# Kernel optimization log

Measured on AMD Instinct MI355X. Metric: run time of the kernel, lower is better.

## Reference

```python
import jax, jax.numpy as jnp
import numpy as np

EPS = 1e-5
QMAX = 127.0


def fake_quant_int8(x):
    """Per-tensor symmetric int8 fake-quant (quantize+dequantize), dynamic scale.
    Mirrors brevitas Int8ActPerTensorFloat / Int8WeightPerTensorFloat math."""
    scale = jnp.maximum(jnp.max(jnp.abs(x)) / QMAX, 1e-8)
    q = jnp.clip(jnp.round(x / scale), -128.0, 127.0) * scale
    # straight-through estimator (identity grad through quant)
    return x + jax.lax.stop_gradient(q - x)


def layer_norm(x, g, b):
    mu = jnp.mean(x, axis=-1, keepdims=True)
    var = jnp.mean(jnp.square(x - mu), axis=-1, keepdims=True)
    return (x - mu) * jax.lax.rsqrt(var + EPS) * g + b


def setup_inputs() -> dict:
    key = jax.random.key(0)
    B, S, D, H = 64, 196, 768, 12
    M = 4 * D
    ks = jax.random.split(key, 8)
    s = lambda d: 1.0 / np.sqrt(d)
    return {
        "x": jax.random.normal(ks[0], (B, S, D), jnp.float32),
        "ln1_g": jnp.ones((D,), jnp.float32),
        "ln1_b": jnp.zeros((D,), jnp.float32),
        "ln2_g": jnp.ones((D,), jnp.float32),
        "ln2_b": jnp.zeros((D,), jnp.float32),
        "w_qkv": jax.random.normal(ks[1], (D, 3 * D), jnp.float32) * s(D),
        "b_qkv": jnp.zeros((3 * D,), jnp.float32),
        "w_o": jax.random.normal(ks[2], (D, D), jnp.float32) * s(D),
        "b_o": jnp.zeros((D,), jnp.float32),
        "w1": jax.random.normal(ks[3], (D, M), jnp.float32) * s(D),
        "b1": jnp.zeros((M,), jnp.float32),
        "w2": jax.random.normal(ks[4], (M, D), jnp.float32) * s(M),
        "b2": jnp.zeros((D,), jnp.float32),
    }


def _block(x, ln1_g, ln1_b, ln2_g, ln2_b, w_qkv, b_qkv, w_o, b_o, w1, b1, w2, b2):
    B, S, D = x.shape
    H = 12
    hd = D // H

    # --- LN -> quant -> MHSA -> add ---
    r1 = x
    h = fake_quant_int8(layer_norm(x, ln1_g, ln1_b))
    qkv = jnp.einsum("bsd,de->bse", h, fake_quant_int8(w_qkv)) + b_qkv
    q, k, v = jnp.split(qkv, 3, axis=-1)
    q = q.reshape(B, S, H, hd)
    k = k.reshape(B, S, H, hd)
    v = v.reshape(B, S, H, hd)
    logits = jnp.einsum("bqhd,bkhd->bhqk", q, k) / jnp.sqrt(jnp.float32(hd))
    attn = jax.nn.softmax(logits, axis=-1)
    ctx = jnp.einsum("bhqk,bkhd->bqhd", attn, v).reshape(B, S, D)
    ctx = fake_quant_int8(ctx)
    mhsa = jnp.einsum("bsd,de->bse", ctx, fake_quant_int8(w_o)) + b_o
    x = mhsa + r1

    # --- LN -> quant -> MLP (fc1 -> GELU -> quant -> fc2) -> add ---
    r2 = x
    h = fake_quant_int8(layer_norm(x, ln2_g, ln2_b))
    h = jnp.einsum("bsd,dm->bsm", h, fake_quant_int8(w1)) + b1
    h = jax.nn.gelu(h, approximate=False)  # torch nn.GELU default = exact erf
    h = fake_quant_int8(h)
    h = jnp.einsum("bsm,md->bsd", h, fake_quant_int8(w2)) + b2
    return h + r2


def reference(x, ln1_g, ln1_b, ln2_g, ln2_b, w_qkv, b_qkv, w_o, b_o, w1, b1, w2, b2):
    return _block(x, ln1_g, ln1_b, ln2_g, ln2_b, w_qkv, b_qkv, w_o, b_o, w1, b1, w2, b2)
```

## Files before the change

### kernel.cpp

```cpp
#include <hip/hip_runtime.h>
#include <cstdint>
#include <cstddef>

#define DEVFN __device__ __forceinline__

typedef short bf16x8 __attribute__((ext_vector_type(8)));
typedef float f32x4  __attribute__((ext_vector_type(4)));
typedef int   i32x4  __attribute__((ext_vector_type(4)));

static constexpr int NTOK  = 64 * 196;
static constexpr int DMODEL= 768;
static constexpr int NHEAD = 12;
static constexpr int NQKV  = 2304;
static constexpr int MMLP  = 3072;
static constexpr int SEQ   = 196;
static constexpr int NBATCH= 64;

enum { SL_LN1=0, SL_WQKV=1, SL_CTX=2, SL_WO=3, SL_LN2=4, SL_W1=5, SL_GELU=6, SL_W2=7 };

static constexpr int NSH       = 64;
static constexpr int SH_STRIDE = 64;
static constexpr int SLOTS_U32 = NSH * SH_STRIDE;

DEVFN float bf2f(unsigned short u){ return __uint_as_float(((unsigned)u) << 16); }
DEVFN unsigned cvt_pk_bf16(float a, float b){
  unsigned r;
  asm("v_cvt_pk_bf16_f32 %0, %1, %2" : "=v"(r) : "v"(a), "v"(b));
  return r;
}
DEVFN void split_pk(float a, float b, unsigned& hp, unsigned& lp){
  hp = cvt_pk_bf16(a, b);
  float ra = a - __uint_as_float(hp << 16);
  float rb = b - __uint_as_float(hp & 0xffff0000u);
  lp = cvt_pk_bf16(ra, rb);
}
DEVFN float slot_absmax(const unsigned* __restrict__ slots, int slot){
  unsigned m = 0u;
#pragma unroll
  for (int j = 0; j < NSH; j++){
    unsigned u = slots[j * SH_STRIDE + slot];
    m = (u > m) ? u : m;
  }
  return __uint_as_float(m);
}
DEVFN float slot_scale(const unsigned* __restrict__ slots, int slot){
  return fmaxf(slot_absmax(slots, slot) / 127.0f, 1e-8f);
}
DEVFN void scatter_amax(unsigned* slots, int slot, unsigned bucket, float v){
  atomicMax(slots + (bucket & (NSH - 1)) * SH_STRIDE + slot, __float_as_uint(v));
}
DEVFN float quantval(float x, float s){
  float q = rintf(x / s);
  return fminf(fmaxf(q, -128.0f), 127.0f);
}
DEVFN unsigned pack4(float a, float b, float c, float d){
  return  ((unsigned)(unsigned char)(char)(int)a)
        | ((unsigned)(unsigned char)(char)(int)b << 8)
        | ((unsigned)(unsigned char)(char)(int)c << 16)
        | ((unsigned)(unsigned char)(char)(int)d << 24);
}
DEVFN float gelu_fast(float v){
  float s  = v * 0.70710678118654752f;
  float ax = fabsf(s);
  float t  = __builtin_amdgcn_rcpf(fmaf(0.3275911f, ax, 1.0f));
  float p  = t * fmaf(t, fmaf(t, fmaf(t, fmaf(t, 1.061405429f, -1.453152027f),
                                      1.421413741f), -0.284496736f), 0.254829592f);
  float er = fmaf(-p, __expf(-ax * ax), 1.0f);
  unsigned sgn = __float_as_uint(s) & 0x80000000u;
  er = __uint_as_float(__float_as_uint(er) | sgn);
  return 0.5f * v * (1.0f + er);
}
DEVFN f32x4 mfma16(bf16x8 a, bf16x8 b, f32x4 c){
  return __builtin_amdgcn_mfma_f32_16x16x32_bf16(a, b, c, 0, 0, 0);
}
DEVFN i32x4 mfma16i8(i32x4 a, i32x4 b, i32x4 c){
  return __builtin_amdgcn_mfma_i32_16x16x64_i8(a, b, c, 0, 0, 0);
}
DEVFN void async_ld16(const void* g, void* lds){
  __builtin_amdgcn_global_load_lds((const __attribute__((address_space(1))) void*)g,
                                   (__attribute__((address_space(3))) void*)lds, 16, 0, 0);
}
DEVFN int vidx(int d, int s){
  return d * 256 + (s ^ (((d ^ (d >> 2)) & 7) << 3));
}
DEVFN void xcd_swizzle(int gx, int gy, int& bx, int& by){
  int nwg = gx * gy;
  int bid = blockIdx.y * gx + blockIdx.x;
  int q = nwg >> 3, r = nwg & 7;
  int xcd = bid & 7, loc = bid >> 3;
  int sw = (xcd < r) ? (xcd * (q + 1) + loc) : (r * (q + 1) + (xcd - r) * q + loc);
  bx = sw % gx; by = sw / gx;
}

DEVFN float ln_stats_wave(const float* __restrict__ x, const float* __restrict__ g,
                          const float* __restrict__ b, float2* __restrict__ stats,
                          int row, int lane){
  const float4* xr = (const float4*)(x + (size_t)row * DMODEL);
  float4 v[3];
  float sum = 0.f;
#pragma unroll
  for (int i = 0; i < 3; i++){ v[i] = xr[i * 64 + lane]; sum += v[i].x + v[i].y + v[i].z + v[i].w; }
  for (int off = 32; off; off >>= 1) sum += __shfl_xor(sum, off);
  float mu = sum * (1.0f / 768.0f);
  float vs = 0.f;
#pragma unroll
  for (int i = 0; i < 3; i++){
    float dx = v[i].x - mu, dy = v[i].y - mu, dz = v[i].z - mu, dw = v[i].w - mu;
    vs += dx * dx + dy * dy + dz * dz + dw * dw;
  }
  for (int off = 32; off; off >>= 1) vs += __shfl_xor(vs, off);
  float inv = 1.0f / sqrtf(vs * (1.0f / 768.0f) + 1e-5f);
  const float4* g4 = (const float4*)g; const float4* b4 = (const float4*)b;
  float am = 0.f;
#pragma unroll
  for (int i = 0; i < 3; i++){
    float4 gg = g4[i * 64 + lane], bb = b4[i * 64 + lane];
    float ox = (v[i].x - mu) * inv * gg.x + bb.x;
    float oy = (v[i].y - mu) * inv * gg.y + bb.y;
    float oz = (v[i].z - mu) * inv * gg.z + bb.z;
    float ow = (v[i].w - mu) * inv * gg.w + bb.w;
    am = fmaxf(am, fmaxf(fmaxf(fabsf(ox), fabsf(oy)), fmaxf(fabsf(oz), fabsf(ow))));
  }
  if (lane == 0) stats[row] = float2{mu, inv};
  return am;
}
DEVFN void ln_quant_wave(const float* __restrict__ x, const float* __restrict__ g,
                         const float* __restrict__ b, const float2* __restrict__ stats,
                         char* __restrict__ outq, float s, int row, int lane){
  float2 st = stats[row];
  float mu = st.x, inv = st.y;
  const float4* xr = (const float4*)(x + (size_t)row * DMODEL);
  const float4* g4 = (const float4*)g; const float4* b4 = (const float4*)b;
  unsigned* oq = (unsigned*)(outq + (size_t)row * DMODEL);
#pragma unroll
  for (int i = 0; i < 3; i++){
    float4 v = xr[i * 64 + lane];
    float4 gg = g4[i * 64 + lane], bb = b4[i * 64 + lane];
    float ox = (v.x - mu) * inv * gg.x + bb.x;
    float oy = (v.y - mu) * inv * gg.y + bb.y;
    float oz = (v.z - mu) * inv * gg.z + bb.z;
    float ow = (v.w - mu) * inv * gg.w + bb.w;
    oq[i * 64 + lane] = pack4(quantval(ox, s), quantval(oy, s),
                              quantval(oz, s), quantval(ow, s));
  }
}

__global__ void k_ln_stats(const float* __restrict__ x, const float* __restrict__ g,
                           const float* __restrict__ b, float2* __restrict__ stats,
                           unsigned* slots, int slot){
  int w = threadIdx.x >> 6, lane = threadIdx.x & 63;
  int row = blockIdx.x * 4 + w;
  float am = ln_stats_wave(x, g, b, stats, row, lane);
  for (int off = 32; off; off >>= 1) am = fmaxf(am, __shfl_xor(am, off));
  __shared__ float am4[4];
  if (lane == 0) am4[w] = am;
  __syncthreads();
  if (threadIdx.x == 0){
    float bm = fmaxf(fmaxf(am4[0], am4[1]), fmaxf(am4[2], am4[3]));
    scatter_amax(slots, slot, blockIdx.x, bm);
  }
}
__global__ void k_ln_quant(const float* __restrict__ x, const float* __restrict__ g,
                           const float* __restrict__ b, const float2* __restrict__ stats,
                           char* __restrict__ outq, const unsigned* __restrict__ slots, int slot){
  int w = threadIdx.x >> 6, lane = threadIdx.x & 63;
  int row = blockIdx.x * 4 + w;
  float s = slot_scale(slots, slot);
  ln_quant_wave(x, g, b, stats, outq, s, row, lane);
}

__global__ void k_prep1(const float* __restrict__ w_qkv, const float* __restrict__ w_o,
                        const float* __restrict__ w1, const float* __restrict__ w2,
                        const float* __restrict__ x, const float* __restrict__ g,
                        const float* __restrict__ b, float2* __restrict__ stats,
                        unsigned* slots){
  __shared__ float red[4];
  int bid = blockIdx.x;
  int lane = threadIdx.x & 63, w = threadIdx.x >> 6;
  if (bid < 896){
    const float* xx; int n4, slot, b0, nb;
    if (bid < 256)      { xx = w_qkv; n4 = DMODEL * NQKV  / 4; slot = SL_WQKV; b0 = 0;   nb = 256; }
    else if (bid < 384) { xx = w_o;   n4 = DMODEL * DMODEL/ 4; slot = SL_WO;   b0 = 256; nb = 128; }
    else if (bid < 640) { xx = w1;    n4 = DMODEL * MMLP  / 4; slot = SL_W1;   b0 = 384; nb = 256; }
    else                { xx = w2;    n4 = MMLP   * DMODEL/ 4; slot = SL_W2;   b0 = 640; nb = 256; }
    int lb = bid - b0;
    float m = 0.f;
    const float4* x4 = (const float4*)xx;
    int stride = nb * blockDim.x;
    for (int j = lb * blockDim.x + threadIdx.x; j < n4; j += stride){
      float4 v = x4[j];
      m = fmaxf(m, fmaxf(fmaxf(fabsf(v.x), fabsf(v.y)), fmaxf(fabsf(v.z), fabsf(v.w))));
    }
    for (int off = 32; off; off >>= 1) m = fmaxf(m, __shfl_xor(m, off));
    if (lane == 0) red[w] = m;
    __syncthreads();
    if (threadIdx.x == 0){
      float bm = fmaxf(fmaxf(red[0], red[1]), fmaxf(red[2], red[3]));
      scatter_amax(slots, slot, bid, bm);
    }
  } else {
    int row = (bid - 896) * 4 + w;
    float am = ln_stats_wave(x, g, b, stats, row, lane);
    for (int off = 32; off; off >>= 1) am = fmaxf(am, __shfl_xor(am, off));
    if (lane == 0) red[w] = am;
    __syncthreads();
    if (threadIdx.x == 0){
      float bm = fmaxf(fmaxf(red[0], red[1]), fmaxf(red[2], red[3]));
      scatter_amax(slots, SL_LN1, bid, bm);
    }
  }
}

__global__ void k_prep2(const float* __restrict__ w0, const float* __restrict__ w1,
                        const float* __restrict__ w2, const float* __restrict__ w3,
                        char* __restrict__ t0, char* __restrict__ t1,
                        char* __restrict__ t2, char* __restrict__ t3,
                        const float* __restrict__ x, const float* __restrict__ g,
                        const float* __restrict__ b, const float2* __restrict__ stats,
                        char* __restrict__ outq, const unsigned* __restrict__ slots){
  __shared__ float tile[32][33];
  int bid = blockIdx.x;
  if (bid < 6912){
    const float* w; char* wt; int K, N, slot, lb;
    if (bid < 1728)      { w = w0; wt = t0; K = DMODEL; N = NQKV;   slot = SL_WQKV; lb = bid; }
    else if (bid < 2304) { w = w1; wt = t1; K = DMODEL; N = DMODEL; slot = SL_WO;   lb = bid - 1728; }
    else if (bid < 4608) { w = w2; wt = t2; K = DMODEL; N = MMLP;   slot = SL_W1;   lb = bid - 2304; }
    else                 { w = w3; wt = t3; K = MMLP;   N = DMODEL; slot = SL_W2;   lb = bid - 4608; }
    int nx = N / 32;
    int bx = lb % nx, by = lb / nx;
    float s = slot_scale(slots, slot);
    int n0 = bx * 32, k0 = by * 32;
    int tx = threadIdx.x & 31, ty = threadIdx.x >> 5;
#pragma unroll
    for (int i = 0; i < 4; i++){
      int k = k0 + ty + i * 8;
      float v = w[(size_t)k * N + n0 + tx];
      tile[ty + i * 8][tx] = quantval(v, s);
    }
    __syncthreads();
    int n = threadIdx.x >> 3, kg = threadIdx.x & 7;
    unsigned o = pack4(tile[kg * 4 + 0][n], tile[kg * 4 + 1][n],
                       tile[kg * 4 + 2][n], tile[kg * 4 + 3][n]);
    *(unsigned*)(wt + (size_t)(n0 + n) * K + k0 + kg * 4) = o;
  } else {
    int w = threadIdx.x >> 6, lane = threadIdx.x & 63;
    int row = (bid - 6912) * 4 + w;
    float s = slot_scale(slots, SL_LN1);
    ln_quant_wave(x, g, b, stats, outq, s, row, lane);
  }
}

__global__ void k_quant_act(const float* __restrict__ x, unsigned* __restrict__ out,
                            int n4, const unsigned* __restrict__ slots, int slot){
  float s = slot_scale(slots, slot);
  const float4* x4 = (const float4*)x;
  int stride = gridDim.x * blockDim.x;
  for (int j = blockIdx.x * blockDim.x + threadIdx.x; j < n4; j += stride){
    float4 v = x4[j];
    out[j] = pack4(quantval(v.x, s), quantval(v.y, s), quantval(v.z, s), quantval(v.w, s));
  }
}

__global__ void k_quant_bf16_i8(const unsigned short* __restrict__ x, unsigned* __restrict__ out,
                                int n4, const unsigned* __restrict__ slots, int slot){
  float s = slot_scale(slots, slot);
  const ushort4* x4 = (const ushort4*)x;
  int stride = gridDim.x * blockDim.x;
  for (int j = blockIdx.x * blockDim.x + threadIdx.x; j < n4; j += stride){
    ushort4 v = x4[j];
    out[j] = pack4(quantval(bf2f(v.x), s), quantval(bf2f(v.y), s),
                   quantval(bf2f(v.z), s), quantval(bf2f(v.w), s));
  }
}

template<int EPI>
__launch_bounds__(256, 4)
__global__ void k_gemm(const char* __restrict__ A,
                       const char* __restrict__ Bt,
                       const float* __restrict__ bias,
                       const float* __restrict__ res,
                       float* __restrict__ Cf,
                       unsigned short* __restrict__ Cb,
                       const unsigned* __restrict__ slots, int sa_slot, int sb_slot,
                       unsigned* gmax_slots, int gmax_slot,
                       int M, int N, int K)
{
  __shared__ __align__(16) char smem[32768];
  __shared__ float gm4[4];
  const int tid  = threadIdx.x;
  const int lane = tid & 63;
  const int wv   = tid >> 6;
  const int wx   = wv & 1, wy = wv >> 1;
  const int quad = lane >> 4;
  const int l16  = lane & 15;
  int bx, by;
  xcd_swizzle(gridDim.x, gridDim.y, bx, by);
  const int m0 = by * 128, n0 = bx * 128;

  auto issue = [&](int k0, int buf){
#pragma unroll
    for (int i = 0; i < 2; i++){
      int c = tid + i * 256;
      int row = c >> 2, q = c & 3;
      int qs = (q - ((row + (row >> 2)) & 3)) & 3;
      async_ld16(A + (size_t)(m0 + row) * K + k0 + qs * 16,
                 smem + buf * 8192 + (i * 256 + wv * 64) * 16);
    }
#pragma unroll
    for (int i = 0; i < 2; i++){
      int c = tid + i * 256;
      int row = c >> 2, q = c & 3;
      int qs = (q - ((row + (row >> 2)) & 3)) & 3;
      async_ld16(Bt + (size_t)(n0 + row) * K + k0 + qs * 16,
                 smem + 16384 + buf * 8192 + (i * 256 + wv * 64) * 16);
    }
  };

  i32x4 acc[4][4] = {};
  const int nk = K >> 6;
  issue(0, 0);

  const int ch = (((quad + (l16 & 3) + (l16 >> 2)) & 3)) * 16;

  for (int k = 0; k < nk; k++){
    const int cur = k & 1;
    if (k + 1 < nk){
      issue((k + 1) << 6, cur ^ 1);
      asm volatile("s_waitcnt vmcnt(4)" ::: "memory");
    } else {
      asm volatile("s_waitcnt vmcnt(0)" ::: "memory");
    }
    asm volatile("s_barrier" ::: "memory");

    const char* Ab = smem + cur * 8192;
    const char* Bb = smem + 16384 + cur * 8192;
    i32x4 af[4], bfr[4];
#pragma unroll
    for (int i = 0; i < 4; i++)
      af[i] = *(const i32x4*)(Ab + (wy * 64 + i * 16 + l16) * 64 + ch);
#pragma unroll
    for (int j = 0; j < 4; j++)
      bfr[j] = *(const i32x4*)(Bb + (wx * 64 + j * 16 + l16) * 64 + ch);
    asm volatile("s_waitcnt lgkmcnt(0)" ::: "memory");
    asm volatile("s_barrier" ::: "memory");

#pragma unroll
    for (int i = 0; i < 4; i++)
#pragma unroll
      for (int j = 0; j < 4; j++)
        acc[i][j] = mfma16i8(af[i], bfr[j], acc[i][j]);
  }
  __syncthreads();

  float (*stage)[132] = (float (*)[132])smem;
  const float sc = slot_scale(slots, sa_slot) * slot_scale(slots, sb_slot);
  const int col4 = (tid & 31) * 4;
  const int gc   = n0 + col4;
  const float4 bb = *(const float4*)&bias[gc];
  float gmax = 0.f;
#pragma unroll
  for (int i = 0; i < 4; i++){
#pragma unroll
    for (int j = 0; j < 4; j++)
#pragma unroll
      for (int r = 0; r < 4; r++)
        stage[wy * 16 + quad * 4 + r][wx * 64 + j * 16 + l16] = (float)acc[i][j][r];
    __syncthreads();
#pragma unroll
    for (int rr = 0; rr < 4; rr++){
      const int rl = rr * 8 + (tid >> 5);
      const int gm = m0 + ((rl >> 4) * 64) + i * 16 + (rl & 15);
      float4 v = *(const float4*)&stage[rl][col4];
      v.x = v.x * sc + bb.x; v.y = v.y * sc + bb.y;
      v.z = v.z * sc + bb.z; v.w = v.w * sc + bb.w;
      if constexpr (EPI == 1){
        float4 rv = *(const float4*)&res[(size_t)gm * N + gc];
        v.x += rv.x; v.y += rv.y; v.z += rv.z; v.w += rv.w;
        *(float4*)&Cf[(size_t)gm * N + gc] = v;
      } else if constexpr (EPI == 2){
        float g0 = gelu_fast(v.x);
        float g1 = gelu_fast(v.y);
        float g2 = gelu_fast(v.z);
        float g3 = gelu_fast(v.w);
        gmax = fmaxf(gmax, fmaxf(fmaxf(fabsf(g0), fabsf(g1)), fmaxf(fabsf(g2), fabsf(g3))));
        uint2 o = {cvt_pk_bf16(g0, g1), cvt_pk_bf16(g2, g3)};
        *(uint2*)&Cb[(size_t)gm * N + gc] = o;
      } else {
        *(float4*)&Cf[(size_t)gm * N + gc] = v;
      }
    }
    __syncthreads();
  }
  if constexpr (EPI == 2){
    for (int off = 32; off; off >>= 1) gmax = fmaxf(gmax, __shfl_xor(gmax, off));
    if (lane == 0) gm4[wv] = gmax;
    __syncthreads();
    if (tid == 0){
      float bm = fmaxf(fmaxf(gm4[0], gm4[1]), fmaxf(gm4[2], gm4[3]));
      scatter_amax(gmax_slots, gmax_slot, blockIdx.x + blockIdx.y * gridDim.x, bm);
    }
  }
}

__launch_bounds__(832, 4)
__global__ void k_attention(const float* __restrict__ qkv, float* __restrict__ ctx,
                            unsigned* slots){
  __shared__ __align__(16) unsigned short Khi[208 * 72], Klo[208 * 72];
  __shared__ __align__(16) unsigned short Vhi[64 * 256], Vlo[64 * 256];
  __shared__ __align__(16) unsigned short Ps[13][2][16 * 40];
  __shared__ float gm[13];

  const int bh = ((blockIdx.x & 7) * 96) + (blockIdx.x >> 3);
  const int b = bh / NHEAD, h = bh % NHEAD;
  const float* base = qkv + (size_t)b * SEQ * NQKV;
  const int tid = threadIdx.x, lane = tid & 63, wv = tid >> 6;
  const int quad = lane >> 4, l16 = lane & 15;

  float4 kreg[4], vreg[5];
#pragma unroll
  for (int i = 0; i < 4; i++){
    int idx = tid + i * 832;
    int r = idx >> 4, c4 = (idx & 15) * 4;
    float4 v = {0.f, 0.f, 0.f, 0.f};
    if (r < SEQ) v = *(const float4*)(base + (size_t)r * NQKV + DMODEL + h * 64 + c4);
    kreg[i] = v;
  }
#pragma unroll
  for (int i = 0; i < 5; i++){
    int idx = tid + i * 832;
    int s = idx >> 4, dg = (idx & 15) * 4;
    float4 v = {0.f, 0.f, 0.f, 0.f};
    if (idx < 232 * 16 && s < SEQ)
      v = *(const float4*)(base + (size_t)s * NQKV + 2 * DMODEL + h * 64 + dg);
    vreg[i] = v;
  }
#pragma unroll
  for (int i = 0; i < 4; i++){
    int idx = tid + i * 832;
    int r = idx >> 4, c4 = (idx & 15) * 4;
    float4 v = kreg[i];
    unsigned h01, l01, h23, l23;
    split_pk(v.x, v.y, h01, l01);
    split_pk(v.z, v.w, h23, l23);
    *(uint2*)(Khi + r * 72 + c4) = uint2{h01, h23};
    *(uint2*)(Klo + r * 72 + c4) = uint2{l01, l23};
  }
#pragma unroll
  for (int i = 0; i < 5; i++){
    int idx = tid + i * 832;
    if (idx < 232 * 16){
      int s = idx >> 4, dg = (idx & 15) * 4;
      float4 v = vreg[i];
      unsigned h01, l01, h23, l23;
      split_pk(v.x, v.y, h01, l01);
      split_pk(v.z, v.w, h23, l23);
      Vhi[vidx(dg + 0, s)] = (unsigned short)h01; Vhi[vidx(dg + 1, s)] = (unsigned short)(h01 >> 16);
      Vhi[vidx(dg + 2, s)] = (unsigned short)h23; Vhi[vidx(dg + 3, s)] = (unsigned short)(h23 >> 16);
      Vlo[vidx(dg + 0, s)] = (unsigned short)l01; Vlo[vidx(dg + 1, s)] = (unsigned short)(l01 >> 16);
      Vlo[vidx(dg + 2, s)] = (unsigned short)l23; Vlo[vidx(dg + 3, s)] = (unsigned short)(l23 >> 16);
    }
  }
  __syncthreads();

  unsigned short* PsH = &Ps[wv][0][0];
  unsigned short* PsL = &Ps[wv][1][0];

  float gmax = 0.f;
  const int qt = wv;
  {
    const int q0 = qt * 16;
    const int sq = q0 + l16;
    const bool valid = sq < SEQ;

    bf16x8 aqh[2], aql[2];
    const float* qrow = base + (size_t)(valid ? sq : 0) * NQKV + h * 64;
#pragma unroll
    for (int ks = 0; ks < 2; ks++){
      float4 v0 = {0,0,0,0}, v1 = {0,0,0,0};
      if (valid){
        v0 = *(const float4*)(qrow + ks * 32 + quad * 8);
        v1 = *(const float4*)(qrow + ks * 32 + quad * 8 + 4);
      }
      unsigned* ah = (unsigned*)&aqh[ks];
      unsigned* al = (unsigned*)&aql[ks];
      split_pk(v0.x, v0.y, ah[0], al[0]);
      split_pk(v0.z, v0.w, ah[1], al[1]);
      split_pk(v1.x, v1.y, ah[2], al[2]);
      split_pk(v1.z, v1.w, ah[3], al[3]);
    }

    f32x4 sacc[13];
    __builtin_amdgcn_s_setprio(1);
#pragma unroll
    for (int t = 0; t < 13; t++){
      f32x4 a = {0.f, 0.f, 0.f, 0.f};
#pragma unroll
      for (int ks = 0; ks < 2; ks++){
        bf16x8 bkh = *(const bf16x8*)(Khi + (t * 16 + l16) * 72 + ks * 32 + quad * 8);
        bf16x8 bkl = *(const bf16x8*)(Klo + (t * 16 + l16) * 72 + ks * 32 + quad * 8);
        a = mfma16(aqh[ks], bkh, a);
        a = mfma16(aqh[ks], bkl, a);
        a = mfma16(aql[ks], bkh, a);
      }
      sacc[t] = a;
    }
    __builtin_amdgcn_s_setprio(0);

    float mx[4] = {-1e30f, -1e30f, -1e30f, -1e30f};
#pragma unroll
    for (int t = 0; t < 13; t++){
      bool dead = (t == 12) && (l16 >= 4);
#pragma unroll
      for (int r = 0; r < 4; r++){
        float v = dead ? -1e30f : sacc[t][r] * 0.125f;
        sacc[t][r] = v;
        mx[r] = fmaxf(mx[r], v);
      }
    }
#pragma unroll
    for (int off = 1; off < 16; off <<= 1)
#pragma unroll
      for (int r = 0; r < 4; r++) mx[r] = fmaxf(mx[r], __shfl_xor(mx[r], off));
    float sum[4] = {0.f, 0.f, 0.f, 0.f};
#pragma unroll
    for (int t = 0; t < 13; t++)
#pragma unroll
      for (int r = 0; r < 4; r++){
        float e = __expf(sacc[t][r] - mx[r]);
        sacc[t][r] = e; sum[r] += e;
      }
#pragma unroll
    for (int off = 1; off < 16; off <<= 1)
#pragma unroll
      for (int r = 0; r < 4; r++) sum[r] += __shfl_xor(sum[r], off);
    float inv[4];
#pragma unroll
    for (int r = 0; r < 4; r++) inv[r] = 1.0f / sum[r];

    f32x4 oacc[4] = {};
#pragma unroll
    for (int ks = 0; ks < 7; ks++){
      const int t0 = 2 * ks, t1 = 2 * ks + 1;
#pragma unroll
      for (int r = 0; r < 4; r++){
        int row = quad * 4 + r;
        float a = sacc[t0][r] * inv[r];
        float c = (t1 < 13) ? sacc[t1][r] * inv[r] : 0.f;
        unsigned hp, lp;
        split_pk(a, c, hp, lp);
        PsH[row * 40 + l16]      = (unsigned short)hp;
        PsH[row * 40 + 16 + l16] = (unsigned short)(hp >> 16);
        PsL[row * 40 + l16]      = (unsigned short)lp;
        PsL[row * 40 + 16 + l16] = (unsigned short)(lp >> 16);
      }
      __builtin_amdgcn_wave_barrier();
      bf16x8 aph = *(const bf16x8*)(PsH + l16 * 40 + quad * 8);
      bf16x8 apl = *(const bf16x8*)(PsL + l16 * 40 + quad * 8);
      __builtin_amdgcn_s_setprio(1);
#pragma unroll
      for (int n = 0; n < 4; n++){
        bf16x8 bvh = *(const bf16x8*)(Vhi + vidx(n * 16 + l16, ks * 32 + quad * 8));
        bf16x8 bvl = *(const bf16x8*)(Vlo + vidx(n * 16 + l16, ks * 32 + quad * 8));
        oacc[n] = mfma16(aph, bvh, oacc[n]);
        oacc[n] = mfma16(aph, bvl, oacc[n]);
        oacc[n] = mfma16(apl, bvh, oacc[n]);
      }
      __builtin_amdgcn_s_setprio(0);
      __builtin_amdgcn_wave_barrier();
    }

#pragma unroll
    for (int r = 0; r < 4; r++){
      int srow = q0 + quad * 4 + r;
      if (srow < SEQ){
#pragma unroll
        for (int n = 0; n < 4; n++){
          float v = oacc[n][r];
          ctx[((size_t)(b * SEQ + srow)) * DMODEL + h * 64 + n * 16 + l16] = v;
          gmax = fmaxf(gmax, fabsf(v));
        }
      }
    }
  }
  for (int off = 32; off; off >>= 1) gmax = fmaxf(gmax, __shfl_xor(gmax, off));
  if (lane == 0) gm[wv] = gmax;
  __syncthreads();
  if (tid == 0){
    float bm = 0.f;
#pragma unroll
    for (int i = 0; i < 13; i++) bm = fmaxf(bm, gm[i]);
    scatter_amax(slots, SL_CTX, blockIdx.x, bm);
  }
}

extern "C" void kernel_launch(void* const* d_in, const int* in_sizes, int n_in,
                              void* d_out, int out_size, void* d_ws, size_t ws_size,
                              hipStream_t stream)
{
  const float* x     = (const float*)d_in[0];
  const float* ln1_g = (const float*)d_in[1];
  const float* ln1_b = (const float*)d_in[2];
  const float* ln2_g = (const float*)d_in[3];
  const float* ln2_b = (const float*)d_in[4];
  const float* w_qkv = (const float*)d_in[5];
  const float* b_qkv = (const float*)d_in[6];
  const float* w_o   = (const float*)d_in[7];
  const float* b_o   = (const float*)d_in[8];
  const float* w1    = (const float*)d_in[9];
  const float* b1    = (const float*)d_in[10];
  const float* w2    = (const float*)d_in[11];
  const float* b2    = (const float*)d_in[12];

  char* ws = (char*)d_ws;
  size_t off = 0;
  unsigned* slots = (unsigned*)ws;                 off += SLOTS_U32 * 4;
  float2* stats = (float2*)(ws + off);             off += (size_t)NTOK * 8;
  char* wqkvT = (char*)(ws + off); off += (size_t)NQKV  * DMODEL;
  char* woT   = (char*)(ws + off); off += (size_t)DMODEL* DMODEL;
  char* w1T   = (char*)(ws + off); off += (size_t)MMLP  * DMODEL;
  char* w2T   = (char*)(ws + off); off += (size_t)DMODEL* MMLP;
  off = (off + 255) & ~(size_t)255;
  float* t1    = (float*)(ws + off);               off += (size_t)NTOK * DMODEL * 4;
  char*  t1q   = (char*)(ws + off);                off += (size_t)NTOK * DMODEL;
  off = (off + 255) & ~(size_t)255;
  float* qkv   = (float*)(ws + off);               off += (size_t)NTOK * NQKV * 4;
  float* xmid  = (float*)(ws + off);               off += (size_t)NTOK * DMODEL * 4;
  unsigned short* h1 = (unsigned short*)qkv;
  char* h1q = (char*)qkv + (size_t)NTOK * MMLP * 2;
  float* outp = (float*)d_out;

  hipMemsetAsync(slots, 0, SLOTS_U32 * 4, stream);

  k_prep1<<<4032, 256, 0, stream>>>(w_qkv, w_o, w1, w2, x, ln1_g, ln1_b, stats, slots);
  k_prep2<<<10048, 256, 0, stream>>>(w_qkv, w_o, w1, w2, wqkvT, woT, w1T, w2T,
                                     x, ln1_g, ln1_b, stats, t1q, slots);

  k_gemm<0><<<dim3(NQKV / 128, NTOK / 128), 256, 0, stream>>>(
      t1q, wqkvT, b_qkv, nullptr, qkv, nullptr, slots, SL_LN1, SL_WQKV, nullptr, 0,
      NTOK, NQKV, DMODEL);

  k_attention<<<NBATCH * NHEAD, 832, 0, stream>>>(qkv, t1, slots);
  {
    int n4 = NTOK * DMODEL / 4;
    k_quant_act<<<2048, 256, 0, stream>>>(t1, (unsigned*)t1q, n4, slots, SL_CTX);
  }
  k_gemm<1><<<dim3(DMODEL / 128, NTOK / 128), 256, 0, stream>>>(
      t1q, woT, b_o, x, xmid, nullptr, slots, SL_CTX, SL_WO, nullptr, 0,
      NTOK, DMODEL, DMODEL);

  k_ln_stats<<<NTOK / 4, 256, 0, stream>>>(xmid, ln2_g, ln2_b, stats, slots, SL_LN2);
  k_ln_quant<<<NTOK / 4, 256, 0, stream>>>(xmid, ln2_g, ln2_b, stats, t1q, slots, SL_LN2);

  k_gemm<2><<<dim3(MMLP / 128, NTOK / 128), 256, 0, stream>>>(
      t1q, w1T, b1, nullptr, nullptr, h1, slots, SL_LN2, SL_W1, slots, SL_GELU,
      NTOK, MMLP, DMODEL);
  {
    int n4 = NTOK * MMLP / 4;
    k_quant_bf16_i8<<<2048, 256, 0, stream>>>(h1, (unsigned*)h1q, n4, slots, SL_GELU);
  }
  k_gemm<1><<<dim3(DMODEL / 128, NTOK / 128), 256, 0, stream>>>(
      h1q, w2T, b2, xmid, outp, nullptr, slots, SL_GELU, SL_W2, nullptr, 0,
      NTOK, DMODEL, MMLP);
}
```

Baseline: 432.8 us.

## Fuse activation int8 quantization into GEMM A-operand load path

Removes the two standalone quantization kernels (fp32 ctx -> int8 and bf16 GELU output -> int8). The out-projection and fc2 GEMMs now load the raw fp32 or bf16 activations into registers, quantize and pack them to int8, and store them into the swizzled shared-memory A tile, while B is still loaded asynchronously. This saves a full write and re-read of the int8 intermediates and two kernel launches. In exchange the A global reads grow (4x for fp32, 2x for bf16, re-read once per N-tile column), the A path goes through registers instead of async loads, and register pressure rises.

```diff
diff --git a/kernel.cpp b/kernel.cpp
--- a/kernel.cpp
+++ b/kernel.cpp
@@ -250,30 +250,7 @@
   }
 }
 
-__global__ void k_quant_act(const float* __restrict__ x, unsigned* __restrict__ out,
-                            int n4, const unsigned* __restrict__ slots, int slot){
-  float s = slot_scale(slots, slot);
-  const float4* x4 = (const float4*)x;
-  int stride = gridDim.x * blockDim.x;
-  for (int j = blockIdx.x * blockDim.x + threadIdx.x; j < n4; j += stride){
-    float4 v = x4[j];
-    out[j] = pack4(quantval(v.x, s), quantval(v.y, s), quantval(v.z, s), quantval(v.w, s));
-  }
-}
-
-__global__ void k_quant_bf16_i8(const unsigned short* __restrict__ x, unsigned* __restrict__ out,
-                                int n4, const unsigned* __restrict__ slots, int slot){
-  float s = slot_scale(slots, slot);
-  const ushort4* x4 = (const ushort4*)x;
-  int stride = gridDim.x * blockDim.x;
-  for (int j = blockIdx.x * blockDim.x + threadIdx.x; j < n4; j += stride){
-    ushort4 v = x4[j];
-    out[j] = pack4(quantval(bf2f(v.x), s), quantval(bf2f(v.y), s),
-                   quantval(bf2f(v.z), s), quantval(bf2f(v.w), s));
-  }
-}
-
-template<int EPI>
+template<int EPI, int ASRC>
 __launch_bounds__(256, 4)
 __global__ void k_gemm(const char* __restrict__ A,
                        const char* __restrict__ Bt,
@@ -297,7 +274,17 @@
   xcd_swizzle(gridDim.x, gridDim.y, bx, by);
   const int m0 = by * 128, n0 = bx * 128;
 
-  auto issue = [&](int k0, int buf){
+  auto issueB = [&](int k0, int buf){
+#pragma unroll
+    for (int i = 0; i < 2; i++){
+      int c = tid + i * 256;
+      int row = c >> 2, q = c & 3;
+      int qs = (q - ((row + (row >> 2)) & 3)) & 3;
+      async_ld16(Bt + (size_t)(n0 + row) * K + k0 + qs * 16,
+                 smem + 16384 + buf * 8192 + (i * 256 + wv * 64) * 16);
+    }
+  };
+  auto issueA_async = [&](int k0, int buf){
 #pragma unroll
     for (int i = 0; i < 2; i++){
       int c = tid + i * 256;
@@ -306,49 +293,125 @@
       async_ld16(A + (size_t)(m0 + row) * K + k0 + qs * 16,
                  smem + buf * 8192 + (i * 256 + wv * 64) * 16);
     }
-#pragma unroll
-    for (int i = 0; i < 2; i++){
-      int c = tid + i * 256;
-      int row = c >> 2, q = c & 3;
-      int qs = (q - ((row + (row >> 2)) & 3)) & 3;
-      async_ld16(Bt + (size_t)(n0 + row) * K + k0 + qs * 16,
-                 smem + 16384 + buf * 8192 + (i * 256 + wv * 64) * 16);
-    }
   };
 
   i32x4 acc[4][4] = {};
   const int nk = K >> 6;
-  issue(0, 0);
-
   const int ch = (((quad + (l16 & 3) + (l16 >> 2)) & 3)) * 16;
 
-  for (int k = 0; k < nk; k++){
-    const int cur = k & 1;
-    if (k + 1 < nk){
-      issue((k + 1) << 6, cur ^ 1);
-      asm volatile("s_waitcnt vmcnt(4)" ::: "memory");
-    } else {
-      asm volatile("s_waitcnt vmcnt(0)" ::: "memory");
-    }
-    asm volatile("s_barrier" ::: "memory");
-
-    const char* Ab = smem + cur * 8192;
-    const char* Bb = smem + 16384 + cur * 8192;
-    i32x4 af[4], bfr[4];
-#pragma unroll
-    for (int i = 0; i < 4; i++)
-      af[i] = *(const i32x4*)(Ab + (wy * 64 + i * 16 + l16) * 64 + ch);
-#pragma unroll
-    for (int j = 0; j < 4; j++)
-      bfr[j] = *(const i32x4*)(Bb + (wx * 64 + j * 16 + l16) * 64 + ch);
-    asm volatile("s_waitcnt lgkmcnt(0)" ::: "memory");
-    asm volatile("s_barrier" ::: "memory");
-
-#pragma unroll
-    for (int i = 0; i < 4; i++)
+  if constexpr (ASRC == 0){
+    issueA_async(0, 0);
+    issueB(0, 0);
+    for (int k = 0; k < nk; k++){
+      const int cur = k & 1;
+      if (k + 1 < nk){
+        issueA_async((k + 1) << 6, cur ^ 1);
+        issueB((k + 1) << 6, cur ^ 1);
+        asm volatile("s_waitcnt vmcnt(4)" ::: "memory");
+      } else {
+        asm volatile("s_waitcnt vmcnt(0)" ::: "memory");
+      }
+      asm volatile("s_barrier" ::: "memory");
+
+      const char* Ab = smem + cur * 8192;
+      const char* Bb = smem + 16384 + cur * 8192;
+      i32x4 af[4], bfr[4];
+#pragma unroll
+      for (int i = 0; i < 4; i++)
+        af[i] = *(const i32x4*)(Ab + (wy * 64 + i * 16 + l16) * 64 + ch);
 #pragma unroll
       for (int j = 0; j < 4; j++)
-        acc[i][j] = mfma16i8(af[i], bfr[j], acc[i][j]);
+        bfr[j] = *(const i32x4*)(Bb + (wx * 64 + j * 16 + l16) * 64 + ch);
+      asm volatile("s_waitcnt lgkmcnt(0)" ::: "memory");
+      asm volatile("s_barrier" ::: "memory");
+
+#pragma unroll
+      for (int i = 0; i < 4; i++)
+#pragma unroll
+        for (int j = 0; j < 4; j++)
+          acc[i][j] = mfma16i8(af[i], bfr[j], acc[i][j]);
+    }
+  } else {
+    const int arow = tid >> 1, ahalf = tid & 1;
+    const int arot = (arow + (arow >> 2)) & 3;
+    const int aoff0 = arow * 64 + (((2 * ahalf + 0) + arot) & 3) * 16;
+    const int aoff1 = arow * 64 + (((2 * ahalf + 1) + arot) & 3) * 16;
+    const float sa_q = slot_scale(slots, sa_slot);
+    float4 ar1[8];
+    uint4  ar3[4];
+
+    auto loadA = [&](int k0){
+      if constexpr (ASRC == 1){
+        const float* As = (const float*)A + (size_t)(m0 + arow) * K + k0 + ahalf * 32;
+#pragma unroll
+        for (int j = 0; j < 8; j++) ar1[j] = *(const float4*)(As + j * 4);
+      } else {
+        const unsigned short* As = (const unsigned short*)A + (size_t)(m0 + arow) * K + k0 + ahalf * 32;
+#pragma unroll
+        for (int j = 0; j < 4; j++) ar3[j] = *(const uint4*)(As + j * 8);
+      }
+    };
+    auto convertA = [&](int buf){
+      unsigned w[8];
+      if constexpr (ASRC == 1){
+#pragma unroll
+        for (int j = 0; j < 8; j++)
+          w[j] = pack4(quantval(ar1[j].x, sa_q), quantval(ar1[j].y, sa_q),
+                       quantval(ar1[j].z, sa_q), quantval(ar1[j].w, sa_q));
+      } else {
+#pragma unroll
+        for (int j = 0; j < 4; j++){
+          uint4 u = ar3[j];
+          w[2*j+0] = pack4(quantval(bf2f((unsigned short)(u.x & 0xffff)), sa_q),
+                           quantval(bf2f((unsigned short)(u.x >> 16)),   sa_q),
+                           quantval(bf2f((unsigned short)(u.y & 0xffff)), sa_q),
+                           quantval(bf2f((unsigned short)(u.y >> 16)),   sa_q));
+          w[2*j+1] = pack4(quantval(bf2f((unsigned short)(u.z & 0xffff)), sa_q),
+                           quantval(bf2f((unsigned short)(u.z >> 16)),   sa_q),
+                           quantval(bf2f((unsigned short)(u.w & 0xffff)), sa_q),
+                           quantval(bf2f((unsigned short)(u.w >> 16)),   sa_q));
+        }
+      }
+      char* Abuf = smem + buf * 8192;
+      *(uint4*)(Abuf + aoff0) = uint4{w[0], w[1], w[2], w[3]};
+      *(uint4*)(Abuf + aoff1) = uint4{w[4], w[5], w[6], w[7]};
+    };
+
+    loadA(0);
+    issueB(0, 0);
+    for (int k = 0; k < nk; k++){
+      const int cur = k & 1;
+      convertA(cur);
+      const bool more = (k + 1 < nk);
+      if (more){
+        loadA((k + 1) << 6);
+        issueB((k + 1) << 6, cur ^ 1);
+        if constexpr (ASRC == 1) asm volatile("s_waitcnt vmcnt(10)" ::: "memory");
+        else                     asm volatile("s_waitcnt vmcnt(6)"  ::: "memory");
+      } else {
+        asm volatile("s_waitcnt vmcnt(0)" ::: "memory");
+      }
+      asm volatile("s_waitcnt lgkmcnt(0)" ::: "memory");
+      asm volatile("s_barrier" ::: "memory");
+
+      const char* Ab = smem + cur * 8192;
+      const char* Bb = smem + 16384 + cur * 8192;
+      i32x4 af[4], bfr[4];
+#pragma unroll
+      for (int i = 0; i < 4; i++)
+        af[i] = *(const i32x4*)(Ab + (wy * 64 + i * 16 + l16) * 64 + ch);
+#pragma unroll
+      for (int j = 0; j < 4; j++)
+        bfr[j] = *(const i32x4*)(Bb + (wx * 64 + j * 16 + l16) * 64 + ch);
+      asm volatile("s_waitcnt lgkmcnt(0)" ::: "memory");
+      asm volatile("s_barrier" ::: "memory");
+
+#pragma unroll
+      for (int i = 0; i < 4; i++)
+#pragma unroll
+        for (int j = 0; j < 4; j++)
+          acc[i][j] = mfma16i8(af[i], bfr[j], acc[i][j]);
+    }
   }
   __syncthreads();
 
@@ -626,7 +689,6 @@
   float* qkv   = (float*)(ws + off);               off += (size_t)NTOK * NQKV * 4;
   float* xmid  = (float*)(ws + off);               off += (size_t)NTOK * DMODEL * 4;
   unsigned short* h1 = (unsigned short*)qkv;
-  char* h1q = (char*)qkv + (size_t)NTOK * MMLP * 2;
   float* outp = (float*)d_out;
 
   hipMemsetAsync(slots, 0, SLOTS_U32 * 4, stream);
@@ -635,30 +697,24 @@
   k_prep2<<<10048, 256, 0, stream>>>(w_qkv, w_o, w1, w2, wqkvT, woT, w1T, w2T,
                                      x, ln1_g, ln1_b, stats, t1q, slots);
 
-  k_gemm<0><<<dim3(NQKV / 128, NTOK / 128), 256, 0, stream>>>(
+  k_gemm<0, 0><<<dim3(NQKV / 128, NTOK / 128), 256, 0, stream>>>(
       t1q, wqkvT, b_qkv, nullptr, qkv, nullptr, slots, SL_LN1, SL_WQKV, nullptr, 0,
       NTOK, NQKV, DMODEL);
 
   k_attention<<<NBATCH * NHEAD, 832, 0, stream>>>(qkv, t1, slots);
-  {
-    int n4 = NTOK * DMODEL / 4;
-    k_quant_act<<<2048, 256, 0, stream>>>(t1, (unsigned*)t1q, n4, slots, SL_CTX);
-  }
-  k_gemm<1><<<dim3(DMODEL / 128, NTOK / 128), 256, 0, stream>>>(
-      t1q, woT, b_o, x, xmid, nullptr, slots, SL_CTX, SL_WO, nullptr, 0,
+
+  k_gemm<1, 1><<<dim3(DMODEL / 128, NTOK / 128), 256, 0, stream>>>(
+      (const char*)t1, woT, b_o, x, xmid, nullptr, slots, SL_CTX, SL_WO, nullptr, 0,
       NTOK, DMODEL, DMODEL);
 
   k_ln_stats<<<NTOK / 4, 256, 0, stream>>>(xmid, ln2_g, ln2_b, stats, slots, SL_LN2);
   k_ln_quant<<<NTOK / 4, 256, 0, stream>>>(xmid, ln2_g, ln2_b, stats, t1q, slots, SL_LN2);
 
-  k_gemm<2><<<dim3(MMLP / 128, NTOK / 128), 256, 0, stream>>>(
+  k_gemm<2, 0><<<dim3(MMLP / 128, NTOK / 128), 256, 0, stream>>>(
       t1q, w1T, b1, nullptr, nullptr, h1, slots, SL_LN2, SL_W1, slots, SL_GELU,
       NTOK, MMLP, DMODEL);
-  {
-    int n4 = NTOK * MMLP / 4;
-    k_quant_bf16_i8<<<2048, 256, 0, stream>>>(h1, (unsigned*)h1q, n4, slots, SL_GELU);
-  }
-  k_gemm<1><<<dim3(DMODEL / 128, NTOK / 128), 256, 0, stream>>>(
-      h1q, w2T, b2, xmid, outp, nullptr, slots, SL_GELU, SL_W2, nullptr, 0,
+
+  k_gemm<1, 3><<<dim3(DMODEL / 128, NTOK / 128), 256, 0, stream>>>(
+      (const char*)h1, w2T, b2, xmid, outp, nullptr, slots, SL_GELU, SL_W2, nullptr, 0,
       NTOK, DMODEL, MMLP);
 }
```

Result: slower. 635.4 us (+46.8%).
